# Optimization experiments

Measured on AMD Instinct MI355X. Metric: run time of the kernel, lower is better.

Reference implementation:

```python
import jax, jax.numpy as jnp
import numpy as np

STRIDE = 16
RATIOS = (0.5, 1.0, 2.0)
SCALES = (8, 16, 32)
NMS_THRESH = 0.7
NUM_PRE = 12000
NUM_POST = 2000
MIN_SIZE = 16.0


def _all_anchors(feat_h, feat_w):
    # base anchors centered at (stride/2, stride/2), (y1, x1, y2, x2)
    base = []
    for r in RATIOS:
        for s in SCALES:
            h = STRIDE * s * np.sqrt(r)
            w = STRIDE * s * np.sqrt(1.0 / r)
            c = STRIDE / 2.0
            base.append([c - h / 2.0, c - w / 2.0, c + h / 2.0, c + w / 2.0])
    base = np.asarray(base, np.float32)  # (A, 4)
    ys = np.arange(feat_h, dtype=np.float32) * STRIDE
    xs = np.arange(feat_w, dtype=np.float32) * STRIDE
    shift = np.stack(np.meshgrid(ys, xs, indexing='ij'), axis=-1)  # (H, W, 2) = (y, x)
    shift4 = np.concatenate([shift, shift], axis=-1)  # (H, W, 4)
    anchors = shift4[:, :, None, :] + base[None, None, :, :]  # (H, W, A, 4)
    return jnp.asarray(anchors.reshape(-1, 4))


def _conv(x, w, b, padding):
    y = jax.lax.conv_general_dilated(x, w, (1, 1), padding,
                                     dimension_numbers=('NCHW', 'OIHW', 'NCHW'))
    return y + b[None, :, None, None]


def _create_rpn_proposals(locs, scores, anchors, img_h, img_w):
    # box deparameterize (y1,x1,y2,x2 anchors; dy,dx,dh,dw locs)
    ha = anchors[:, 2] - anchors[:, 0]
    wa = anchors[:, 3] - anchors[:, 1]
    cya = anchors[:, 0] + 0.5 * ha
    cxa = anchors[:, 1] + 0.5 * wa
    cy = locs[:, 0] * ha + cya
    cx = locs[:, 1] * wa + cxa
    h = ha * jnp.exp(locs[:, 2])
    w = wa * jnp.exp(locs[:, 3])
    boxes = jnp.stack([cy - 0.5 * h, cx - 0.5 * w, cy + 0.5 * h, cx + 0.5 * w], axis=1)

    order = jnp.argsort(-scores)[:NUM_PRE]
    boxes = boxes[order]
    s = scores[order]

    lim = jnp.array([img_h, img_w, img_h, img_w], dtype=boxes.dtype)
    boxes = jnp.clip(boxes, 0.0, lim)
    valid = ((boxes[:, 2] - boxes[:, 0]) >= MIN_SIZE) & ((boxes[:, 3] - boxes[:, 1]) >= MIN_SIZE)

    areas = (boxes[:, 2] - boxes[:, 0]) * (boxes[:, 3] - boxes[:, 1])
    n = boxes.shape[0]
    idx = jnp.arange(n)

    def body(i, suppressed):
        bi = boxes[i]
        yy1 = jnp.maximum(bi[0], boxes[:, 0])
        xx1 = jnp.maximum(bi[1], boxes[:, 1])
        yy2 = jnp.minimum(bi[2], boxes[:, 2])
        xx2 = jnp.minimum(bi[3], boxes[:, 3])
        inter = jnp.maximum(yy2 - yy1, 0.0) * jnp.maximum(xx2 - xx1, 0.0)
        iou = inter / (areas[i] + areas - inter + 1e-10)
        new_sup = suppressed | ((iou > NMS_THRESH) & (idx > i))
        return jnp.where(suppressed[i], suppressed, new_sup)

    suppressed = jax.lax.fori_loop(0, n, body, ~valid)
    keep = (~suppressed) & valid
    rank = jnp.cumsum(keep) - 1
    tgt = jnp.where(keep & (rank < NUM_POST), rank, NUM_POST)  # overflow slot
    out = jnp.zeros((NUM_POST + 1, 4), boxes.dtype).at[tgt].set(boxes)[:NUM_POST]
    return out  # (2000, 4), zero-padded if fewer kept


def setup_inputs() -> dict:
    key = jax.random.key(0)
    ks = jax.random.split(key, 7)
    in_c, out_c, A = 1024, 512, 9
    x = jax.random.normal(ks[0], (1, in_c, 64, 64), dtype=jnp.float32)
    conv_w = jax.random.normal(ks[1], (out_c, in_c, 3, 3), jnp.float32) * 0.01
    conv_b = jnp.zeros((out_c,), jnp.float32)
    score_w = jax.random.normal(ks[2], (A * 2, out_c, 1, 1), jnp.float32) * 0.01
    score_b = jnp.zeros((A * 2,), jnp.float32)
    loc_w = jax.random.normal(ks[3], (A * 4, out_c, 1, 1), jnp.float32) * 0.01
    loc_b = jnp.zeros((A * 4,), jnp.float32)
    return {"x": x, "conv_w": conv_w, "conv_b": conv_b,
            "score_w": score_w, "score_b": score_b,
            "loc_w": loc_w, "loc_b": loc_b,
            "img_h": 1024, "img_w": 1024}


def reference(x, conv_w, conv_b, score_w, score_b, loc_w, loc_b, img_h, img_w):
    _, _, fh, fw = x.shape
    anchors = _all_anchors(fh, fw)  # (fh*fw*A, 4)
    h = jax.nn.leaky_relu(_conv(x, conv_w, conv_b, 'SAME'), 0.01)
    rpn_locs = _conv(h, loc_w, loc_b, 'VALID').transpose(0, 2, 3, 1).reshape(-1, 4)
    rpn_scores = _conv(h, score_w, score_b, 'VALID').transpose(0, 2, 3, 1).reshape(-1, 2)
    fg = jax.nn.softmax(rpn_scores, axis=1)[:, 1]
    rois = _create_rpn_proposals(jax.lax.stop_gradient(rpn_locs),
                                 jax.lax.stop_gradient(fg),
                                 anchors, img_h, img_w)
    return rpn_locs, rpn_scores, rois, anchors
```

## Files before the change

kernel.cpp:

```cpp
#include <hip/hip_runtime.h>
#include <cstdint>
#include <cstddef>
#include <math.h>

#define NANCH    36864
#define NPRE     12000
#define NPRE_PAD 12032
#define NW       188
#define SORT_N   16384
#define NPOST    2000

typedef double d4_t __attribute__((ext_vector_type(4)));

__device__ __forceinline__ int tribase(int ci) { return ci * NW - (ci * (ci - 1)) / 2; }

__global__ __launch_bounds__(256, 2)
void k_conv_mfma(const float* __restrict__ xg, const float* __restrict__ wg_,
                 const float* __restrict__ bg, float* __restrict__ hg)
{
    __shared__ __align__(16) float wlds[36 * 64 * 4];
    __shared__ __align__(16) float xlds[16 * 3 * 68];
    const int tid = threadIdx.x;
    const int oct = blockIdx.x & 7;
    const int y   = blockIdx.x >> 3;
    const int oc0 = oct << 6;
    const int l   = tid & 63;
    const int wv  = tid >> 6;
    const int g   = l >> 4;
    const int li  = l & 15;
    const int wm  = wv >> 1;
    const int wn  = wv & 1;

    int pr[4], qc[4];
    int aG = g;
    {
        d4_t Pz = {0., 0., 0., 0.}, Qz = {0., 0., 0., 0.}, Tz = {0., 0., 0., 0.};
        Pz = __builtin_amdgcn_mfma_f64_16x16x4f64((double)li, 1.0, Pz, 0, 0, 0);
        Qz = __builtin_amdgcn_mfma_f64_16x16x4f64(1.0, (double)li, Qz, 0, 0, 0);
        Tz = __builtin_amdgcn_mfma_f64_16x16x4f64((double)g, (double)(1 << (2 * g)),
                                                  Tz, 0, 0, 0);
        bool ok = true;
        const int tval = (int)Tz[0];
        if ((int)Tz[1] != tval || (int)Tz[2] != tval || (int)Tz[3] != tval) ok = false;
        int seen = 0;
#pragma unroll
        for (int j = 0; j < 4; ++j) {
            int d = (tval >> (2 * j)) & 3;
            seen |= 1 << d;
            if (d == g) aG = j;
        }
        if (seen != 15) ok = false;
#pragma unroll
        for (int r = 0; r < 4; ++r) {
            int pv = (int)Pz[r], qv = (int)Qz[r];
            if ((pv & 3) || (qv & 3)) ok = false;
            pr[r] = pv >> 2; qc[r] = qv >> 2;
            if (pr[r] > 15 || qc[r] > 15) ok = false;
        }
        if (!ok) {
#pragma unroll
            for (int r = 0; r < 4; ++r) { pr[r] = 4 * g + r; qc[r] = li; }
            aG = g;
        }
    }

    d4_t acc00 = {0., 0., 0., 0.}, acc01 = {0., 0., 0., 0.};
    d4_t acc10 = {0., 0., 0., 0.}, acc11 = {0., 0., 0., 0.};

    int xoff[13], loff[13];
#pragma unroll
    for (int t = 0; t < 13; ++t) {
        int f = tid + 256 * t;
        if (f < 3168) {
            int ic = f / 198; int r = f - ic * 198; int sr = r / 66; int gc = r - sr * 66;
            loff[t] = (ic * 3 + sr) * 68 + gc;
            int gy = y + sr - 1, gx = gc - 1;
            xoff[t] = (gy >= 0 && gy < 64 && gx >= 0 && gx < 64)
                      ? (ic * 4096 + gy * 64 + gx) : -1;
        } else { loff[t] = -1; xoff[t] = -1; }
    }

    const float* wptr = wg_ + (size_t)(oc0 + l) * 9216 + 4 * wv;
    float4 wr[9];
    float  xr[13];
#pragma unroll
    for (int i = 0; i < 9; ++i) wr[i] = *(const float4*)(wptr + 16 * i);
#pragma unroll
    for (int t = 0; t < 13; ++t) xr[t] = (xoff[t] >= 0) ? xg[xoff[t]] : 0.f;

    const int abase = wm * 32 + li;
    const int bbase = (wn * 32 + li) * 4 + g;

#pragma unroll 1
    for (int cc = 0; cc < 64; ++cc) {
        __syncthreads();
#pragma unroll
        for (int i = 0; i < 9; ++i)
            *(float4*)&wlds[((wv + 4 * i) * 64 + l) * 4] = wr[i];
#pragma unroll
        for (int t = 0; t < 13; ++t)
            if (loff[t] >= 0) xlds[loff[t]] = xr[t];
        if (cc < 63) {
            const float* wp = wptr + (cc + 1) * 144;
            const float* xp = xg + (size_t)(cc + 1) * 65536;
#pragma unroll
            for (int i = 0; i < 9; ++i) wr[i] = *(const float4*)(wp + 16 * i);
#pragma unroll
            for (int t = 0; t < 13; ++t) xr[t] = (xoff[t] >= 0) ? xp[xoff[t]] : 0.f;
        }
        __syncthreads();
#pragma unroll
        for (int s = 0; s < 36; ++s) {
            int k   = 4 * s + aG;
            int icL = k / 9; int tap = k - 9 * icL;
            int ky  = tap / 3; int kx = tap - 3 * ky;
            int ax  = (icL * 3 + ky) * 68 + kx + abase;
            double a0 = (double)xlds[ax];
            double a1 = (double)xlds[ax + 16];
            double b0 = (double)wlds[bbase + s * 256];
            double b1 = (double)wlds[bbase + s * 256 + 64];
            acc00 = __builtin_amdgcn_mfma_f64_16x16x4f64(a0, b0, acc00, 0, 0, 0);
            acc01 = __builtin_amdgcn_mfma_f64_16x16x4f64(a0, b1, acc01, 0, 0, 0);
            acc10 = __builtin_amdgcn_mfma_f64_16x16x4f64(a1, b0, acc10, 0, 0, 0);
            acc11 = __builtin_amdgcn_mfma_f64_16x16x4f64(a1, b1, acc11, 0, 0, 0);
        }
    }

    __syncthreads();
    float* olds = wlds;
    {
#pragma unroll
        for (int r = 0; r < 4; ++r) {
            const int oca = wn * 32 + qc[r];
            const int ocb = oca + 16;
            const double ba = (double)bg[oc0 + oca];
            const double bb = (double)bg[oc0 + ocb];
            const int pxa = wm * 32 + pr[r];
            const int pxb = pxa + 16;
            double t00 = acc00[r] + ba;
            double t01 = acc01[r] + bb;
            double t10 = acc10[r] + ba;
            double t11 = acc11[r] + bb;
            olds[oca * 68 + pxa] = (float)((t00 >= 0.0) ? t00 : 0.01 * t00);
            olds[ocb * 68 + pxa] = (float)((t01 >= 0.0) ? t01 : 0.01 * t01);
            olds[oca * 68 + pxb] = (float)((t10 >= 0.0) ? t10 : 0.01 * t10);
            olds[ocb * 68 + pxb] = (float)((t11 >= 0.0) ? t11 : 0.01 * t11);
        }
    }
    __syncthreads();
    {
        const int oc = tid >> 2, q = tid & 3;
        float* dst = hg + (size_t)(oc0 + oc) * 4096 + y * 64 + q * 16;
        const float* src = &olds[oc * 68 + q * 16];
#pragma unroll
        for (int j = 0; j < 4; ++j)
            *(float4*)(dst + 4 * j) = *(const float4*)(src + 4 * j);
    }
}

__global__ __launch_bounds__(256, 1)
void k_heads(const float* __restrict__ hg, const float* __restrict__ loc_w,
             const float* __restrict__ loc_b, const float* __restrict__ score_w,
             const float* __restrict__ score_b, const int* __restrict__ imh,
             const int* __restrict__ imw, float* __restrict__ out,
             float* __restrict__ boxes_all, unsigned long long* __restrict__ keys64)
{
    __shared__ float  hch[64 * 64];
    __shared__ float  wch[54 * 64];
    __shared__ float  ol[54 * 64];
    __shared__ double sld[18 * 64];
    const int y = blockIdx.x, tid = threadIdx.x;
    const int px = tid & 63, cg = tid >> 6;
    double acc[14];
#pragma unroll
    for (int u = 0; u < 14; ++u) acc[u] = 0.0;
    for (int cc = 0; cc < 8; ++cc) {
        __syncthreads();
#pragma unroll
        for (int t = 0; t < 16; ++t) {
            int f = tid + 256 * t;
            hch[f] = hg[(size_t)(cc * 64 + (f >> 6)) * 4096 + y * 64 + (f & 63)];
        }
#pragma unroll
        for (int t = 0; t < 14; ++t) {
            int f = tid + 256 * t;
            if (f < 54 * 64) {
                int ch = f >> 6, c = f & 63;
                wch[f] = (ch < 36) ? loc_w[ch * 512 + cc * 64 + c]
                                   : score_w[(ch - 36) * 512 + cc * 64 + c];
            }
        }
        __syncthreads();
        for (int c = 0; c < 64; ++c) {
            double hvd = (double)hch[c * 64 + px];
#pragma unroll
            for (int u = 0; u < 14; ++u) {
                int ch = cg + 4 * u;
                if (ch < 54) acc[u] = fma((double)wch[ch * 64 + c], hvd, acc[u]);
            }
        }
    }
    __syncthreads();
#pragma unroll
    for (int u = 0; u < 14; ++u) {
        int ch = cg + 4 * u;
        if (ch < 54) {
            double s = acc[u] + (double)((ch < 36) ? loc_b[ch] : score_b[ch - 36]);
            ol[ch * 64 + px] = (float)s;
            if (ch >= 36) sld[(ch - 36) * 64 + px] = s;
        }
    }
    __syncthreads();
    for (int f = tid; f < 64 * 36; f += 256) {
        int p = f / 36, ch = f - 36 * p;
        out[(size_t)(y * 64 + p) * 36 + ch] = ol[ch * 64 + p];
    }
    for (int f = tid; f < 64 * 18; f += 256) {
        int p = f / 18, ch = f - 18 * p;
        out[147456 + (size_t)(y * 64 + p) * 18 + ch] = ol[(36 + ch) * 64 + p];
    }
    const float fy = (float)(*imh), fx = (float)(*imw);
    float* anch = out + 229184;
    for (int t2 = tid; t2 < 576; t2 += 256) {
        int p = t2 / 9, a = t2 - 9 * p;
        int pg = y * 64 + p;
        int ar = a / 3, as = a - 3 * ar;
        double rr = (ar == 0) ? 0.5 : ((ar == 1) ? 1.0 : 2.0);
        double ss = (as == 0) ? 8.0 : ((as == 1) ? 16.0 : 32.0);
        double hh = 16.0 * ss * sqrt(rr), wwd = 16.0 * ss * sqrt(1.0 / rr);
        float by1 = (float)(8.0 - hh * 0.5), bx1 = (float)(8.0 - wwd * 0.5);
        float by2 = (float)(8.0 + hh * 0.5), bx2 = (float)(8.0 + wwd * 0.5);
        float sy = (float)(y * 16), sx = (float)(p * 16);
        float a0 = sy + by1, a1 = sx + bx1, a2 = sy + by2, a3 = sx + bx2;
        int base = (pg * 9 + a) * 4;
        anch[base + 0] = a0; anch[base + 1] = a1; anch[base + 2] = a2; anch[base + 3] = a3;
        double d = sld[(a * 2 + 1) * 64 + p] - sld[(a * 2) * 64 + p];
        long long bits = __double_as_longlong(d);
        unsigned long long u64 =
            (unsigned long long)(bits ^ ((bits >> 63) | (long long)0x8000000000000000LL));
        unsigned long long v = ~u64;
        keys64[pg * 9 + a] = (v & 0xFFFFFFFFFFFF0000ULL) | (unsigned long long)(pg * 9 + a);
        float dy = ol[(a * 4 + 0) * 64 + p], dxv = ol[(a * 4 + 1) * 64 + p];
        float dh = ol[(a * 4 + 2) * 64 + p], dwv = ol[(a * 4 + 3) * 64 + p];
        float hA = a2 - a0, wA = a3 - a1;
        float cya = a0 + 0.5f * hA, cxa = a1 + 0.5f * wA;
        float cy = dy * hA + cya, cx = dxv * wA + cxa;
        float hb = hA * expf(dh), wb = wA * expf(dwv);
        float b0 = fminf(fmaxf(cy - 0.5f * hb, 0.f), fy);
        float b1 = fminf(fmaxf(cx - 0.5f * wb, 0.f), fx);
        float b2 = fminf(fmaxf(cy + 0.5f * hb, 0.f), fy);
        float b3 = fminf(fmaxf(cx + 0.5f * wb, 0.f), fx);
        boxes_all[base + 0] = b0; boxes_all[base + 1] = b1;
        boxes_all[base + 2] = b2; boxes_all[base + 3] = b3;
    }
}

__global__ __launch_bounds__(1024, 1)
void k_select(const unsigned long long* __restrict__ keys64,
              const float* __restrict__ boxes_all,
              unsigned long long* __restrict__ sortbuf, float* __restrict__ sbox,
              float* __restrict__ areas, unsigned long long* __restrict__ suppr)
{
    __shared__ unsigned int hist[256];
    __shared__ unsigned int sh_below, sh_prefix, sh_nsel;
    __shared__ unsigned long long tile[4096];
    const int tid = threadIdx.x;
    if (tid == 0) { sh_below = 0; sh_prefix = 0; sh_nsel = 0; }
    __syncthreads();
    for (int p = 3; p >= 0; --p) {
        if (tid < 256) hist[tid] = 0;
        __syncthreads();
        unsigned int pref = sh_prefix;
        int shift = p * 8;
        for (int i = tid; i < NANCH; i += 1024) {
            unsigned int k = (unsigned int)(keys64[i] >> 32);
            bool match = (p == 3) || ((k >> (shift + 8)) == pref);
            if (match) atomicAdd(&hist[(k >> shift) & 255u], 1u);
        }
        __syncthreads();
        if (tid == 0) {
            unsigned int below = sh_below, cacc = 0;
            int b = 0;
            for (; b < 256; ++b) {
                if (below + cacc + hist[b] >= NPRE) break;
                cacc += hist[b];
            }
            if (b > 255) b = 255;
            sh_below = below + cacc;
            sh_prefix = (pref << 8) | (unsigned int)b;
        }
        __syncthreads();
    }
    const unsigned int P = sh_prefix;
    for (int i = tid; i < NANCH; i += 1024) {
        unsigned long long k = keys64[i];
        if ((unsigned int)(k >> 32) <= P) {
            unsigned int pos = atomicAdd(&sh_nsel, 1u);
            if (pos < SORT_N) sortbuf[pos] = k;
        }
    }
    __syncthreads();
    unsigned int nsel = sh_nsel; if (nsel > SORT_N) nsel = SORT_N;
    for (unsigned int i = nsel + tid; i < SORT_N; i += 1024) sortbuf[i] = ~0ULL;
    __syncthreads();
    for (int T = 0; T < 4; ++T) {
        for (int t = tid; t < 4096; t += 1024) tile[t] = sortbuf[T * 4096 + t];
        __syncthreads();
        for (int k2 = 2; k2 <= 4096; k2 <<= 1) {
            for (int j = k2 >> 1; j > 0; j >>= 1) {
                for (int t = tid; t < 2048; t += 1024) {
                    int i = ((t & ~(j - 1)) << 1) | (t & (j - 1));
                    int ip = i | j;
                    bool up = (((T * 4096 + i) & k2) == 0);
                    unsigned long long A = tile[i], B = tile[ip];
                    if ((A > B) == up) { tile[i] = B; tile[ip] = A; }
                }
                __syncthreads();
            }
        }
        for (int t = tid; t < 4096; t += 1024) sortbuf[T * 4096 + t] = tile[t];
        __syncthreads();
    }
    auto gstage = [&](int k2, int j) {
        for (int t = tid; t < 8192; t += 1024) {
            int i = ((t & ~(j - 1)) << 1) | (t & (j - 1));
            int ip = i | j;
            bool up = ((i & k2) == 0);
            unsigned long long A = sortbuf[i], B = sortbuf[ip];
            if ((A > B) == up) { sortbuf[i] = B; sortbuf[ip] = A; }
        }
        __syncthreads();
    };
    auto ltail = [&](int k2) {
        for (int T = 0; T < 4; ++T) {
            for (int t = tid; t < 4096; t += 1024) tile[t] = sortbuf[T * 4096 + t];
            __syncthreads();
            for (int j = 2048; j > 0; j >>= 1) {
                for (int t = tid; t < 2048; t += 1024) {
                    int i = ((t & ~(j - 1)) << 1) | (t & (j - 1));
                    int ip = i | j;
                    bool up = (((T * 4096 + i) & k2) == 0);
                    unsigned long long A = tile[i], B = tile[ip];
                    if ((A > B) == up) { tile[i] = B; tile[ip] = A; }
                }
                __syncthreads();
            }
            for (int t = tid; t < 4096; t += 1024) sortbuf[T * 4096 + t] = tile[t];
            __syncthreads();
        }
    };
    gstage(8192, 4096);  ltail(8192);
    gstage(16384, 8192); gstage(16384, 4096); ltail(16384);

    if (tid < NW) suppr[tid] = (tid == NW - 1) ? 0xFFFFFFFF00000000ULL : 0ULL;
    __syncthreads();
    for (int r = tid; r < NPRE_PAD; r += 1024) {
        float b0 = 0, b1 = 0, b2 = 0, b3 = 0;
        if (r < NPRE) {
            unsigned int idx = (unsigned int)(sortbuf[r] & 0xFFFFULL);
            const float* bp = boxes_all + (size_t)idx * 4;
            b0 = bp[0]; b1 = bp[1]; b2 = bp[2]; b3 = bp[3];
        }
        sbox[r * 4 + 0] = b0; sbox[r * 4 + 1] = b1;
        sbox[r * 4 + 2] = b2; sbox[r * 4 + 3] = b3;
        areas[r] = (b2 - b0) * (b3 - b1);
        if (r < NPRE) {
            bool valid = ((b2 - b0) >= 16.0f) && ((b3 - b1) >= 16.0f);
            if (!valid) atomicOr(&suppr[r >> 6], 1ULL << (r & 63));
        }
    }
}

__global__ __launch_bounds__(256, 1)
void k_mask(const float* __restrict__ sbox, const float* __restrict__ areas,
            unsigned long long* __restrict__ mask)
{
    const int cj = blockIdx.x, q = blockIdx.y;
    __shared__ float4 bx[64];
    __shared__ float aj[64];
    const int t = threadIdx.x;
    const int j0 = cj * 64;
    if (t < 64) { bx[t] = ((const float4*)sbox)[j0 + t]; aj[t] = areas[j0 + t]; }
    __syncthreads();
    const int c0 = ((cj + 1) * q) >> 2, c1 = ((cj + 1) * (q + 1)) >> 2;
    for (int i0 = c0 * 64; i0 < c1 * 64; i0 += 256) {
        int i = i0 + t;
        if (i < c1 * 64) {
            const float4 p = ((const float4*)sbox)[i];
            const float ai = areas[i];
            unsigned long long w = 0;
            for (int jj = 0; jj < 64; ++jj) {
                float4 qb = bx[jj];
                float yy1 = fmaxf(p.x, qb.x), xx1 = fmaxf(p.y, qb.y);
                float yy2 = fminf(p.z, qb.z), xx2 = fminf(p.w, qb.w);
                float inter = fmaxf(yy2 - yy1, 0.f) * fmaxf(xx2 - xx1, 0.f);
                float iou = inter / (ai + aj[jj] - inter + 1e-10f);
                w |= ((unsigned long long)((iou > 0.7f) && (j0 + jj > i))) << jj;
            }
            int ci = i >> 6;
            mask[(size_t)(tribase(ci) + (cj - ci)) * 64 + (i & 63)] = w;
        }
    }
}

__global__ __launch_bounds__(256, 1)
void k_scan(const unsigned long long* __restrict__ mask,
            const unsigned long long* __restrict__ suppr,
            const float* __restrict__ sbox, float* __restrict__ rois)
{
    __shared__ unsigned long long rvs[NW];
    __shared__ unsigned long long curw;
    __shared__ unsigned long long keptw[NW];
    __shared__ int totkept, brk;
    __shared__ int pref[NW + 1];
    const int tid = threadIdx.x;
    if (tid < NW) { rvs[tid] = suppr[tid]; keptw[tid] = 0ULL; }
    if (tid == 0) { totkept = 0; brk = 0; }
    __syncthreads();
    for (int c = 0; c < NW; ++c) {
        if (tid < 64) {
            unsigned long long diag = mask[(size_t)tribase(c) * 64 + tid];
            unsigned long long w = rvs[c];
            for (int b = 0; b < 64; ++b) {
                unsigned long long db = __shfl(diag, b, 64);
                if (!((w >> b) & 1ULL)) w |= db;
            }
            if (tid == 0) {
                curw = w;
                keptw[c] = ~w;
                totkept += __popcll(~w);
                if (totkept >= NPOST) brk = 1;
            }
        }
        __syncthreads();
        if (brk) break;
        unsigned long long kw = ~curw;
        if (tid > c && tid < NW) {
            const unsigned long long* mrow = mask + (size_t)(tribase(c) + (tid - c)) * 64;
            unsigned long long a0 = 0, a1 = 0, a2 = 0, a3 = 0;
            for (int b = 0; b < 64; b += 4) {
                unsigned long long m0 = mrow[b + 0];
                unsigned long long m1 = mrow[b + 1];
                unsigned long long m2 = mrow[b + 2];
                unsigned long long m3 = mrow[b + 3];
                if ((kw >> (b + 0)) & 1ULL) a0 |= m0;
                if ((kw >> (b + 1)) & 1ULL) a1 |= m1;
                if ((kw >> (b + 2)) & 1ULL) a2 |= m2;
                if ((kw >> (b + 3)) & 1ULL) a3 |= m3;
            }
            rvs[tid] |= a0 | a1 | a2 | a3;
        }
        __syncthreads();
    }
    __syncthreads();
    if (tid == 0) {
        int s = 0;
        for (int c = 0; c < NW; ++c) { pref[c] = s; s += __popcll(keptw[c]); }
        pref[NW] = s;
    }
    __syncthreads();
    int total = pref[NW]; if (total > NPOST) total = NPOST;
    for (int r = total * 4 + tid; r < NPOST * 4; r += 256) rois[r] = 0.f;
    if (tid < NW) {
        unsigned long long kw = keptw[tid];
        int r = pref[tid];
        for (int b = 0; b < 64; ++b) {
            if ((kw >> b) & 1ULL) {
                if (r < NPOST) {
                    const float* bp = sbox + (size_t)(tid * 64 + b) * 4;
                    rois[r * 4 + 0] = bp[0]; rois[r * 4 + 1] = bp[1];
                    rois[r * 4 + 2] = bp[2]; rois[r * 4 + 3] = bp[3];
                }
                ++r;
            }
        }
    }
}

extern "C" void kernel_launch(void* const* d_in, const int* in_sizes, int n_in,
                              void* d_out, int out_size, void* d_ws, size_t ws_size,
                              hipStream_t stream)
{
    const float* x       = (const float*)d_in[0];
    const float* conv_w  = (const float*)d_in[1];
    const float* conv_b  = (const float*)d_in[2];
    const float* score_w = (const float*)d_in[3];
    const float* score_b = (const float*)d_in[4];
    const float* loc_w   = (const float*)d_in[5];
    const float* loc_b   = (const float*)d_in[6];
    const int*   imh     = (const int*)d_in[7];
    const int*   imw     = (const int*)d_in[8];
    float* out = (float*)d_out;
    char* ws = (char*)d_ws;
    float* h                    = (float*)(ws);
    float* boxes_all            = (float*)(ws + 8388608);
    unsigned long long* keys64  = (unsigned long long*)(ws + 8978432);
    float* sbox                 = (float*)(ws + 9273344);
    float* areas                = (float*)(ws + 9465856);
    unsigned long long* suppr   = (unsigned long long*)(ws + 9513984);
    unsigned long long* sortbuf = (unsigned long long*)(ws + 9515520);
    unsigned long long* mask    = (unsigned long long*)(ws + 9646592);

    k_conv_mfma<<<512, 256, 0, stream>>>(x, conv_w, conv_b, h);
    k_heads <<<64, 256, 0, stream>>>(h, loc_w, loc_b, score_w, score_b, imh, imw,
                                     out, boxes_all, keys64);
    k_select<<<1, 1024, 0, stream>>>(keys64, boxes_all, sortbuf, sbox, areas, suppr);
    k_mask  <<<dim3(188, 4), 256, 0, stream>>>(sbox, areas, mask);
    k_scan  <<<1, 256, 0, stream>>>(mask, suppr, sbox, out + 221184);
}
```

Baseline: 1.800 ms.

## Double-buffer conv LDS tiles with async global-to-LDS weight loads

Restructures the 3x3 conv MFMA main loop into a double-buffered LDS pipeline. Each stage now covers 8 input channels instead of 16, over 128 iterations. Weights go straight from global memory into LDS via global_load_lds, skipping the register round trip, while the next input rows are prefetched into registers. Explicit waitcnt and barrier placement lets the next stage's loads overlap the current stage's MFMAs, at the cost of more barriers per channel and a fragile hand-tuned vmcnt.

Measured after the change: 1.757 ms. 1.02x faster.

```diff
diff --git a/kernel.cpp b/kernel.cpp
--- a/kernel.cpp
+++ b/kernel.cpp
@@ -14,12 +14,19 @@
 
 __device__ __forceinline__ int tribase(int ci) { return ci * NW - (ci * (ci - 1)) / 2; }
 
+typedef __attribute__((address_space(1))) const void* as1cv_t;
+typedef __attribute__((address_space(3))) void* as3v_t;
+__device__ __forceinline__ void gload_lds16(const float* g, float* l)
+{
+    __builtin_amdgcn_global_load_lds((as1cv_t)g, (as3v_t)l, 16, 0, 0);
+}
+
 __global__ __launch_bounds__(256, 2)
 void k_conv_mfma(const float* __restrict__ xg, const float* __restrict__ wg_,
                  const float* __restrict__ bg, float* __restrict__ hg)
 {
-    __shared__ __align__(16) float wlds[36 * 64 * 4];
-    __shared__ __align__(16) float xlds[16 * 3 * 68];
+    __shared__ __align__(16) float wlds[2][4608];
+    __shared__ __align__(16) float xlds[2][1632];
     const int tid = threadIdx.x;
     const int oct = blockIdx.x & 7;
     const int y   = blockIdx.x >> 3;
@@ -67,11 +74,11 @@
     d4_t acc00 = {0., 0., 0., 0.}, acc01 = {0., 0., 0., 0.};
     d4_t acc10 = {0., 0., 0., 0.}, acc11 = {0., 0., 0., 0.};
 
-    int xoff[13], loff[13];
-#pragma unroll
-    for (int t = 0; t < 13; ++t) {
+    int xoff[7], loff[7];
+#pragma unroll
+    for (int t = 0; t < 7; ++t) {
         int f = tid + 256 * t;
-        if (f < 3168) {
+        if (f < 1584) {
             int ic = f / 198; int r = f - ic * 198; int sr = r / 66; int gc = r - sr * 66;
             loff[t] = (ic * 3 + sr) * 68 + gc;
             int gy = y + sr - 1, gx = gc - 1;
@@ -80,54 +87,92 @@
         } else { loff[t] = -1; xoff[t] = -1; }
     }
 
-    const float* wptr = wg_ + (size_t)(oc0 + l) * 9216 + 4 * wv;
-    float4 wr[9];
-    float  xr[13];
-#pragma unroll
-    for (int i = 0; i < 9; ++i) wr[i] = *(const float4*)(wptr + 16 * i);
-#pragma unroll
-    for (int t = 0; t < 13; ++t) xr[t] = (xoff[t] >= 0) ? xg[xoff[t]] : 0.f;
-
+    const float* wsrc0 = wg_ + (size_t)(oc0 + l) * 9216;
     const int abase = wm * 32 + li;
     const int bbase = (wn * 32 + li) * 4 + g;
-
+    float xr[7];
+
+    {
+#pragma unroll
+        for (int i = 0; i < 5; ++i) {
+            int slot = wv + 4 * i;
+            if (slot < 18) gload_lds16(wsrc0 + 4 * slot, &wlds[0][slot * 256]);
+        }
+#pragma unroll
+        for (int t = 0; t < 7; ++t) xr[t] = (xoff[t] >= 0) ? xg[xoff[t]] : 0.f;
+#pragma unroll
+        for (int t = 0; t < 7; ++t)
+            if (loff[t] >= 0) xlds[0][loff[t]] = xr[t];
+        const float* xp = xg + 32768;
+#pragma unroll
+        for (int t = 0; t < 7; ++t) xr[t] = (xoff[t] >= 0) ? xp[xoff[t]] : 0.f;
+        asm volatile("s_waitcnt lgkmcnt(0)" ::: "memory");
+        asm volatile("s_waitcnt vmcnt(0)" ::: "memory");
+        __builtin_amdgcn_sched_barrier(0);
+        __builtin_amdgcn_s_barrier();
+        __builtin_amdgcn_sched_barrier(0);
+    }
+
+    int cur = 0;
 #pragma unroll 1
-    for (int cc = 0; cc < 64; ++cc) {
-        __syncthreads();
-#pragma unroll
-        for (int i = 0; i < 9; ++i)
-            *(float4*)&wlds[((wv + 4 * i) * 64 + l) * 4] = wr[i];
-#pragma unroll
-        for (int t = 0; t < 13; ++t)
-            if (loff[t] >= 0) xlds[loff[t]] = xr[t];
-        if (cc < 63) {
-            const float* wp = wptr + (cc + 1) * 144;
-            const float* xp = xg + (size_t)(cc + 1) * 65536;
-#pragma unroll
-            for (int i = 0; i < 9; ++i) wr[i] = *(const float4*)(wp + 16 * i);
-#pragma unroll
-            for (int t = 0; t < 13; ++t) xr[t] = (xoff[t] >= 0) ? xp[xoff[t]] : 0.f;
-        }
-        __syncthreads();
-#pragma unroll
-        for (int s = 0; s < 36; ++s) {
+    for (int cc = 0; cc < 128; ++cc) {
+        if (cc < 127) {
+            const float* wsrc = wsrc0 + (cc + 1) * 72;
+            float* wdst = &wlds[cur ^ 1][0];
+#pragma unroll
+            for (int i = 0; i < 5; ++i) {
+                int slot = wv + 4 * i;
+                if (slot < 18) gload_lds16(wsrc + 4 * slot, wdst + slot * 256);
+            }
+            __builtin_amdgcn_sched_barrier(0);
+            float* xdst = &xlds[cur ^ 1][0];
+#pragma unroll
+            for (int t = 0; t < 7; ++t)
+                if (loff[t] >= 0) xdst[loff[t]] = xr[t];
+            __builtin_amdgcn_sched_barrier(0);
+            {
+                int nc = (cc + 2 < 128) ? (cc + 2) : 127;
+                const float* xp = xg + (size_t)nc * 32768;
+#pragma unroll
+                for (int t = 0; t < 7; ++t) xr[t] = (xoff[t] >= 0) ? xp[xoff[t]] : 0.f;
+            }
+            __builtin_amdgcn_sched_barrier(0);
+            asm volatile("s_waitcnt lgkmcnt(0)" ::: "memory");
+            asm volatile("s_waitcnt vmcnt(11)" ::: "memory");
+        } else {
+            asm volatile("s_waitcnt lgkmcnt(0)" ::: "memory");
+            asm volatile("s_waitcnt vmcnt(0)" ::: "memory");
+        }
+        __builtin_amdgcn_sched_barrier(0);
+        __builtin_amdgcn_s_barrier();
+        __builtin_amdgcn_sched_barrier(0);
+
+        const float* wb = &wlds[cur][0];
+        const float* xb = &xlds[cur][0];
+#pragma unroll
+        for (int s = 0; s < 18; ++s) {
             int k   = 4 * s + aG;
             int icL = k / 9; int tap = k - 9 * icL;
             int ky  = tap / 3; int kx = tap - 3 * ky;
             int ax  = (icL * 3 + ky) * 68 + kx + abase;
-            double a0 = (double)xlds[ax];
-            double a1 = (double)xlds[ax + 16];
-            double b0 = (double)wlds[bbase + s * 256];
-            double b1 = (double)wlds[bbase + s * 256 + 64];
+            double a0 = (double)xb[ax];
+            double a1 = (double)xb[ax + 16];
+            double b0 = (double)wb[bbase + s * 256];
+            double b1 = (double)wb[bbase + s * 256 + 64];
             acc00 = __builtin_amdgcn_mfma_f64_16x16x4f64(a0, b0, acc00, 0, 0, 0);
             acc01 = __builtin_amdgcn_mfma_f64_16x16x4f64(a0, b1, acc01, 0, 0, 0);
             acc10 = __builtin_amdgcn_mfma_f64_16x16x4f64(a1, b0, acc10, 0, 0, 0);
             acc11 = __builtin_amdgcn_mfma_f64_16x16x4f64(a1, b1, acc11, 0, 0, 0);
         }
-    }
-
-    __syncthreads();
-    float* olds = wlds;
+        __builtin_amdgcn_sched_barrier(0);
+        asm volatile("s_waitcnt lgkmcnt(0)" ::: "memory");
+        __builtin_amdgcn_s_barrier();
+        __builtin_amdgcn_sched_barrier(0);
+        cur ^= 1;
+    }
+
+    __syncthreads();
+    float* olds = &wlds[0][0];
     {
 #pragma unroll
         for (int r = 0; r < 4; ++r) {
```
